# Optimization experiments

Measured on AMD Instinct MI355X. Metric: run time of the kernel, lower is better.

Reference implementation:

```python
import jax, jax.numpy as jnp
import numpy as np

G = 1        # num_dispatch_groups
C = 8        # dispatch_group_size (chips)
EPC = 4      # experts_per_chip
E = 32       # num_routed_experts
K = 8        # num_experts_per_tok
S = 256      # seq_len_per_chip
H = 2048     # hidden_dim
M = 2048     # max_dispatched_tokens_per_expert
ML = 8       # metadata_len
CAP = M // C # per-chip slot region per expert
# expert_dispatch_table: expert e lives on chip e // EPC (all present)
TABLE = jnp.asarray(np.arange(E) // EPC, dtype=jnp.int32)[None, :]  # (G, E)


def setup_inputs() -> dict:
    key = jax.random.key(0)
    k1, k2, k3 = jax.random.split(key, 3)
    x = jax.random.normal(k1, (C, S, H), dtype=jnp.float32)
    weights = jax.random.uniform(k2, (C, S, K), dtype=jnp.float32)
    indices = jax.random.randint(k3, (C, S, K), 0, E).astype(jnp.int32)
    # each source chip writes into its own disjoint slot region per expert
    expert_offsets = jnp.broadcast_to((jnp.arange(C, dtype=jnp.int32) * CAP)[:, None], (C, E))
    return {"x": x, "weights": weights, "indices": indices, "expert_offsets": expert_offsets}


def _dst_slots(indices, expert_offsets):
    """Replicates the sequential offset_copy bookkeeping: dst = base offset +
    number of earlier (token, topk) picks of the same expert on the same chip."""
    idx = indices.reshape(C, S * K)  # flat (token, topk) order matches loop order
    oh = (idx[:, :, None] == jnp.arange(E, dtype=jnp.int32)[None, None, :]).astype(jnp.int32)  # [C, SK, E]
    rank = jnp.take_along_axis(jnp.cumsum(oh, axis=1) - oh, idx[..., None], axis=2)[..., 0]    # [C, SK]
    base = jnp.take_along_axis(expert_offsets, idx, axis=1)                                     # [C, SK]
    return idx, base + rank


def reference(x, weights, indices, expert_offsets):
    idx, dst = _dst_slots(indices, expert_offsets)                 # [C, SK]
    tokens = jnp.arange(S * K, dtype=jnp.int32) // K               # token id per flat pos
    topk = jnp.arange(S * K, dtype=jnp.int32) % K                  # topk id per flat pos
    vals = x[:, tokens]                                            # [C, SK, H] gather
    # bf16 weight bits viewed as int16, sign-extended into int32 (matches torch .view(int16))
    wbits = jax.lax.bitcast_convert_type(weights.astype(jnp.bfloat16), jnp.int16).astype(jnp.int32).reshape(C, S * K)
    chips = jnp.broadcast_to(jnp.arange(C, dtype=jnp.int32)[:, None], (C, S * K))
    meta_rows = jnp.stack(
        [chips, jnp.broadcast_to(tokens, (C, S * K)), jnp.broadcast_to(topk, (C, S * K)), idx, wbits]
        + [jnp.zeros((C, S * K), jnp.int32)] * (ML - 5), axis=-1)  # [C, SK, ML]
    eic = idx % EPC                                                # expert index within chip

    buf = jnp.zeros((G, C, EPC, M, H), dtype=jnp.float32)
    meta = jnp.full((G, C, EPC, M, ML), -1, dtype=jnp.int32)
    for g in range(G):
        ec = TABLE[g][idx]                                         # destination chip per dispatch
        ec = jnp.where(ec >= 0, ec, C)                             # -1 -> out of bounds -> dropped
        f = lambda a: a.reshape(-1)
        buf = buf.at[g, f(ec), f(eic), f(dst)].set(vals.reshape(-1, H), mode='drop')
        meta = meta.at[g, f(ec), f(eic), f(dst)].set(meta_rows.reshape(-1, ML), mode='drop')
    return buf, meta
```

## Files before the change

kernel.cpp:

```cpp
#include <hip/hip_runtime.h>
#include <hip/hip_bf16.h>
#include <stdint.h>

#define C_   8
#define EPC_ 4
#define E_   32
#define K_   8
#define S_   256
#define H_   2048
#define M_   2048
#define ML_  8
#define CAP_ 256
#define SK_  2048
#define NROWS_ (E_ * M_)
#define NREG_  256
#define BUF_ELEMS_ ((size_t)E_ * M_ * H_)
#define SROWS_ 32
#define NSTREAM_ (NROWS_ / SROWS_)
#define NMETA_   NREG_

typedef float f32x4 __attribute__((ext_vector_type(4)));

__global__ __launch_bounds__(64) void rank_kernel(
        const int* __restrict__ indices,
        const int* __restrict__ expert_offsets,
        int* __restrict__ inv,
        int* __restrict__ cnt) {
    const int c    = blockIdx.x >> 5;
    const int e    = blockIdx.x & 31;
    const int lane = threadIdx.x;
    const int* __restrict__ ip = indices + c * SK_;
    const int base = expert_offsets[c * E_ + e];

    int running = 0;
    const unsigned long long below = (lane == 63) ? (~0ULL >> 1)
                                                  : (1ULL << lane) - 1ULL;
    #pragma unroll 4
    for (int ch = 0; ch < SK_ / 64; ++ch) {
        const int i = ch * 64 + lane;
        const bool hit = (ip[i] == e);
        const unsigned long long m = __ballot(hit);
        if (hit) {
            const int dst = base + running + __popcll(m & below);
            if ((unsigned)dst < (unsigned)M_) {
                inv[e * M_ + dst] = c * SK_ + i;
            }
        }
        running += __popcll(m);
    }
    if (lane == 0) cnt[c * E_ + e] = running;
}

__global__ __launch_bounds__(256) void fill_stream(
        const float* __restrict__ x,
        const float* __restrict__ w,
        const int* __restrict__ inv,
        const int* __restrict__ cnt,
        float* __restrict__ buf,
        float* __restrict__ meta) {
    const int t = threadIdx.x;
    const f32x4 z = {0.f, 0.f, 0.f, 0.f};

    if (blockIdx.x < NSTREAM_) {
        const int lb  = blockIdx.x >> 8;
        const int reg = blockIdx.x & 255;
        const int r0  = reg * NREG_ + lb * SROWS_;
        const int e   = reg >> 3;
        const int c   = reg & 7;
        const int slot0 = lb * SROWS_;

        int nocc = cnt[c * E_ + e] - slot0;
        nocc = (nocc < 0) ? 0 : ((nocc > SROWS_) ? SROWS_ : nocc);

        if (nocc > 0) {
            int pp = inv[r0];
            const f32x4* __restrict__ s0 = reinterpret_cast<const f32x4*>(
                x + (size_t)((pp >> 11) * S_ + ((pp & (SK_ - 1)) >> 3)) * H_);
            f32x4 A0 = s0[t];
            f32x4 A1 = s0[t + 256];
            for (int j = 0; j < nocc; ++j) {
                f32x4 B0 = z, B1 = z;
                if (j + 1 < nocc) {
                    const int pn = inv[r0 + j + 1];
                    const f32x4* __restrict__ sn = reinterpret_cast<const f32x4*>(
                        x + (size_t)((pn >> 11) * S_ + ((pn & (SK_ - 1)) >> 3)) * H_);
                    B0 = sn[t];
                    B1 = sn[t + 256];
                }
                f32x4* __restrict__ brow =
                    reinterpret_cast<f32x4*>(buf + (size_t)(r0 + j) * H_);
                __builtin_nontemporal_store(A0, brow + t);
                __builtin_nontemporal_store(A1, brow + t + 256);
                A0 = B0;
                A1 = B1;
            }
        }
        for (int j = nocc; j < SROWS_; ++j) {
            f32x4* __restrict__ brow =
                reinterpret_cast<f32x4*>(buf + (size_t)(r0 + j) * H_);
            __builtin_nontemporal_store(z, brow + t);
            __builtin_nontemporal_store(z, brow + t + 256);
        }
    } else {
        const int reg  = blockIdx.x - NSTREAM_;
        const int e    = reg >> 3;
        const int c    = reg & 7;
        const int cntv = cnt[c * E_ + e];
        f32x4* __restrict__ M4 =
            reinterpret_cast<f32x4*>(meta + (size_t)reg * NREG_ * ML_);

        #pragma unroll
        for (int i0 = 0; i0 < 2; ++i0) {
            const int i    = i0 * 256 + t;
            const int row  = i >> 1;
            const int half = i & 1;
            f32x4 mv;
            if (row < cntv) {
                const int pp    = inv[reg * NREG_ + row];
                const int cc    = pp >> 11;
                const int ii    = pp & (SK_ - 1);
                const int token = ii >> 3;
                const int topk  = ii & (K_ - 1);
                if (half == 0) {
                    mv = (f32x4){(float)cc, (float)token, (float)topk, (float)e};
                } else {
                    const float wv    = w[pp];
                    const uint32_t u  = __float_as_uint(wv);
                    const uint32_t rb = (u + 0x7FFFu + ((u >> 16) & 1u)) >> 16;
                    const int wb      = (int)(short)(unsigned short)rb;
                    mv = (f32x4){(float)wb, 0.f, 0.f, 0.f};
                }
            } else {
                mv = (f32x4){-1.f, -1.f, -1.f, -1.f};
            }
            __builtin_nontemporal_store(mv, M4 + i);
        }
    }
}

extern "C" void kernel_launch(void* const* d_in, const int* in_sizes, int n_in,
                              void* d_out, int out_size, void* d_ws, size_t ws_size,
                              hipStream_t stream) {
    const float* x   = (const float*)d_in[0];
    const float* w   = (const float*)d_in[1];
    const int* idx   = (const int*)d_in[2];
    const int* eo    = (const int*)d_in[3];

    float* buf  = (float*)d_out;
    float* meta = buf + BUF_ELEMS_;

    int* inv = (int*)d_ws;
    int* cnt = inv + NROWS_;

    rank_kernel<<<C_ * E_, 64, 0, stream>>>(idx, eo, inv, cnt);
    fill_stream<<<NSTREAM_ + NMETA_, 256, 0, stream>>>(x, w, inv, cnt, buf, meta);
}
```

Baseline: 114.4 us.

## Split gather-copy and zero-fill into separate balanced block sets

Replaces the per-32-row streaming blocks, which mixed copy and zero work, with two block groups. Copy blocks split each region's occupied rows evenly eight ways, and zero blocks handle 8-row chunks, exiting early when fully occupied. Zero stores switch from nontemporal to regular stores, and the count is clamped to the region size. This aims to balance load, since occupied rows cluster at the start of each region, at the cost of many more tiny blocks.

```diff
diff --git a/kernel.cpp b/kernel.cpp
--- a/kernel.cpp
+++ b/kernel.cpp
@@ -15,8 +15,11 @@
 #define NROWS_ (E_ * M_)
 #define NREG_  256
 #define BUF_ELEMS_ ((size_t)E_ * M_ * H_)
-#define SROWS_ 32
-#define NSTREAM_ (NROWS_ / SROWS_)
+
+#define NCPB_    8
+#define NCOPY_   (NREG_ * NCPB_)
+#define ZROWS_   8
+#define NZERO_   (NROWS_ / ZROWS_)
 #define NMETA_   NREG_
 
 typedef float f32x4 __attribute__((ext_vector_type(4)));
@@ -51,7 +54,7 @@
     if (lane == 0) cnt[c * E_ + e] = running;
 }
 
-__global__ __launch_bounds__(256) void fill_stream(
+__global__ __launch_bounds__(256) void fill_all(
         const float* __restrict__ x,
         const float* __restrict__ w,
         const int* __restrict__ inv,
@@ -61,51 +64,63 @@
     const int t = threadIdx.x;
     const f32x4 z = {0.f, 0.f, 0.f, 0.f};
 
-    if (blockIdx.x < NSTREAM_) {
-        const int lb  = blockIdx.x >> 8;
-        const int reg = blockIdx.x & 255;
-        const int r0  = reg * NREG_ + lb * SROWS_;
-        const int e   = reg >> 3;
-        const int c   = reg & 7;
-        const int slot0 = lb * SROWS_;
+    if (blockIdx.x < NCOPY_) {
+        const int reg  = blockIdx.x >> 3;
+        const int part = blockIdx.x & 7;
+        const int e    = reg >> 3;
+        const int c    = reg & 7;
+
+        int n = cnt[c * E_ + e];
+        n = (n > NREG_) ? NREG_ : n;
+        const int lo = (part * n) >> 3;
+        const int hi = ((part + 1) * n) >> 3;
+        if (lo >= hi) return;
+
+        const int rbase = reg * NREG_;
+        int pp = inv[rbase + lo];
+        const f32x4* __restrict__ s0 = reinterpret_cast<const f32x4*>(
+            x + (size_t)((pp >> 11) * S_ + ((pp & (SK_ - 1)) >> 3)) * H_);
+        f32x4 A0 = s0[t];
+        f32x4 A1 = s0[t + 256];
+        for (int j = lo; j < hi; ++j) {
+            f32x4 B0 = z, B1 = z;
+            if (j + 1 < hi) {
+                const int pn = inv[rbase + j + 1];
+                const f32x4* __restrict__ sn = reinterpret_cast<const f32x4*>(
+                    x + (size_t)((pn >> 11) * S_ + ((pn & (SK_ - 1)) >> 3)) * H_);
+                B0 = sn[t];
+                B1 = sn[t + 256];
+            }
+            f32x4* __restrict__ brow =
+                reinterpret_cast<f32x4*>(buf + (size_t)(rbase + j) * H_);
+            __builtin_nontemporal_store(A0, brow + t);
+            __builtin_nontemporal_store(A1, brow + t + 256);
+            A0 = B0;
+            A1 = B1;
+        }
+    } else if (blockIdx.x < NCOPY_ + NZERO_) {
+        const int r0    = (blockIdx.x - NCOPY_) * ZROWS_;
+        const int e     = r0 >> 11;
+        const int dst0  = r0 & (M_ - 1);
+        const int c     = dst0 >> 8;
+        const int slot0 = dst0 & (CAP_ - 1);
 
         int nocc = cnt[c * E_ + e] - slot0;
-        nocc = (nocc < 0) ? 0 : ((nocc > SROWS_) ? SROWS_ : nocc);
+        if (nocc >= ZROWS_) return;
+        if (nocc < 0) nocc = 0;
 
-        if (nocc > 0) {
-            int pp = inv[r0];
-            const f32x4* __restrict__ s0 = reinterpret_cast<const f32x4*>(
-                x + (size_t)((pp >> 11) * S_ + ((pp & (SK_ - 1)) >> 3)) * H_);
-            f32x4 A0 = s0[t];
-            f32x4 A1 = s0[t + 256];
-            for (int j = 0; j < nocc; ++j) {
-                f32x4 B0 = z, B1 = z;
-                if (j + 1 < nocc) {
-                    const int pn = inv[r0 + j + 1];
-                    const f32x4* __restrict__ sn = reinterpret_cast<const f32x4*>(
-                        x + (size_t)((pn >> 11) * S_ + ((pn & (SK_ - 1)) >> 3)) * H_);
-                    B0 = sn[t];
-                    B1 = sn[t + 256];
-                }
-                f32x4* __restrict__ brow =
-                    reinterpret_cast<f32x4*>(buf + (size_t)(r0 + j) * H_);
-                __builtin_nontemporal_store(A0, brow + t);
-                __builtin_nontemporal_store(A1, brow + t + 256);
-                A0 = B0;
-                A1 = B1;
-            }
-        }
-        for (int j = nocc; j < SROWS_; ++j) {
+        for (int j = nocc; j < ZROWS_; ++j) {
             f32x4* __restrict__ brow =
                 reinterpret_cast<f32x4*>(buf + (size_t)(r0 + j) * H_);
-            __builtin_nontemporal_store(z, brow + t);
-            __builtin_nontemporal_store(z, brow + t + 256);
+            brow[t]       = z;
+            brow[t + 256] = z;
         }
     } else {
-        const int reg  = blockIdx.x - NSTREAM_;
+        const int reg  = blockIdx.x - (NCOPY_ + NZERO_);
         const int e    = reg >> 3;
         const int c    = reg & 7;
-        const int cntv = cnt[c * E_ + e];
+        int cntv = cnt[c * E_ + e];
+        cntv = (cntv > NREG_) ? NREG_ : cntv;
         f32x4* __restrict__ M4 =
             reinterpret_cast<f32x4*>(meta + (size_t)reg * NREG_ * ML_);
 
@@ -153,5 +168,5 @@
     int* cnt = inv + NROWS_;
 
     rank_kernel<<<C_ * E_, 64, 0, stream>>>(idx, eo, inv, cnt);
-    fill_stream<<<NSTREAM_ + NMETA_, 256, 0, stream>>>(x, w, inv, cnt, buf, meta);
+    fill_all<<<NCOPY_ + NZERO_ + NMETA_, 256, 0, stream>>>(x, w, inv, cnt, buf, meta);
 }
```

New measurement: 107.9 us. 5.7% less time.
